# Kernel optimization log

Measured on AMD Instinct MI355X. Metric: run time of the kernel, lower is better.

The kernel has to match this reference:

```python
import jax, jax.numpy as jnp
import numpy as np

B, S, D_IN, H, N_NODES, N_EDGES = 32, 1024, 128, 512, 1024, 16384
SPECTRAL = [0.9, 0.8]   # 0.9 - i*0.1
LEAK = [0.1, 0.15]      # 0.1 + i*0.05
INPUT_SCALING, BIAS_SCALING = 1.0, 0.1


def _make_reservoir(rng, h, radius):
    """Random reservoir matrix with 4-population block scaling, normalized to target spectral radius."""
    W = rng.standard_normal((h, h)).astype(np.float64)
    p = h // 4
    bounds = [0, p, 2 * p, 3 * p, h]
    scales = [(1.2, 0.5), (0.8, 1.3), (1.5, 0.7), (1.0, 1.0)]  # (diag_block, off_block)
    for i in range(4):
        s, e = bounds[i], bounds[i + 1]
        diag, off = scales[i]
        diag_block = W[s:e, s:e] * diag
        W[s:e, :] *= off
        W[s:e, s:e] = diag_block
    ev = np.linalg.eigvals(W)
    W *= radius / np.abs(ev).max()
    return W.astype(np.float32)


def _linear(rng, out_f, in_f):
    k = 1.0 / np.sqrt(in_f)
    Wt = rng.uniform(-k, k, (out_f, in_f)).astype(np.float32)
    b = rng.uniform(-k, k, (out_f,)).astype(np.float32)
    return Wt, b


def setup_inputs() -> dict:
    rng = np.random.default_rng(0)
    x = jnp.asarray(rng.standard_normal((B, S, D_IN)).astype(np.float32))
    edge_index = jnp.asarray(rng.integers(0, N_NODES, (2, N_EDGES)), dtype=jnp.int64)
    inp = {"x": x, "edge_index": edge_index}
    in_sizes = [D_IN, H]
    for l in range(2):
        W_in = (rng.standard_normal((H, in_sizes[l])).astype(np.float32) * INPUT_SCALING)
        W_res = _make_reservoir(rng, H, SPECTRAL[l])
        bias = (rng.standard_normal((H,)).astype(np.float32) * BIAS_SCALING)
        Wp, bp = _linear(rng, N_NODES, H)   # graph_proj: hidden -> num_nodes
        Wu, bu = _linear(rng, H, N_NODES)   # graph_unproj: num_nodes -> hidden
        inp.update({f"W_in{l}": jnp.asarray(W_in), f"W_res{l}": jnp.asarray(W_res),
                    f"bias{l}": jnp.asarray(bias), f"Wp{l}": jnp.asarray(Wp),
                    f"bp{l}": jnp.asarray(bp), f"Wu{l}": jnp.asarray(Wu),
                    f"bu{l}": jnp.asarray(bu)})
    return inp


def _run_layer(x, W_in, W_res, bias, Wp, bp, Wu, bu, src, dst, leak):
    # x: (B, S, D); recurrent scan over time.
    def step(h, x_t):
        inp = x_t @ W_in.T                      # (B, H)
        res = h @ W_res.T                       # (B, H)
        hg = h @ Wp.T + bp                      # (B, N) project onto graph nodes
        # scatter-add message passing: aggr[b, dst] += hg[b, src]
        aggr = jnp.zeros_like(hg).at[:, dst].add(hg[:, src])
        gc = aggr @ Wu.T + bu                   # (B, H)
        h_new = jnp.tanh(inp + res + gc + bias)
        h = (1.0 - leak) * h + leak * h_new     # leaky integration
        return h, h
    h0 = jnp.zeros((x.shape[0], W_res.shape[0]), x.dtype)
    _, ys = jax.lax.scan(step, h0, jnp.swapaxes(x, 0, 1))  # ys: (S, B, H)
    return jnp.swapaxes(ys, 0, 1)


def reference(x, edge_index,
              W_in0, W_res0, bias0, Wp0, bp0, Wu0, bu0,
              W_in1, W_res1, bias1, Wp1, bp1, Wu1, bu1):
    src, dst = edge_index[0], edge_index[1]
    h = _run_layer(x, W_in0, W_res0, bias0, Wp0, bp0, Wu0, bu0, src, dst, LEAK[0])
    h = _run_layer(h, W_in1, W_res1, bias1, Wp1, bp1, Wu1, bu1, src, dst, LEAK[1])
    return h  # dropout is identity in eval mode
```

## Files before the change

### kernel.cpp

```cpp
#include <hip/hip_runtime.h>
#include <hip/hip_bf16.h>
#include <hip/hip_fp16.h>
#include <cstddef>
#include <cstdint>

#define HDIM 512
#define NNODES 1024
#define NEDGES 16384
#define BATCH 32
#define SEQ 1024
#define DIN 128
#define SLICES 8

#define RLX __ATOMIC_RELAXED
#define AGT __HIP_MEMORY_SCOPE_AGENT

typedef _Float16 h2 __attribute__((ext_vector_type(2)));

__global__ void scatter_awp_kernel(const float* __restrict__ Wp,
                                   const int* __restrict__ src,
                                   const int* __restrict__ dst,
                                   float* __restrict__ AWp) {
    int e = blockIdx.x;
    int c = threadIdx.x;
    int s = src[e], d = dst[e];
    atomicAdd(&AWp[d * HDIM + c],       Wp[s * HDIM + c]);
    atomicAdd(&AWp[d * HDIM + 256 + c], Wp[s * HDIM + 256 + c]);
}

__global__ void scatter_abp_kernel(const float* __restrict__ bp,
                                   const int* __restrict__ src,
                                   const int* __restrict__ dst,
                                   float* __restrict__ Abp) {
    int e = blockIdx.x * blockDim.x + threadIdx.x;
    if (e < NEDGES) atomicAdd(&Abp[dst[e]], bp[src[e]]);
}

__global__ void beff_kernel(const float* __restrict__ Wu,
                            const float* __restrict__ Abp,
                            const float* __restrict__ bias,
                            const float* __restrict__ bu,
                            float* __restrict__ beff) {
    int i = threadIdx.x;
    float s = 0.f;
    for (int d = 0; d < NNODES; ++d) s += Wu[i * NNODES + d] * Abp[d];
    beff[i] = bias[i] + bu[i] + s;
}

__global__ void tof16_kernel(const float* __restrict__ in,
                             __half* __restrict__ out, int n) {
    int i = blockIdx.x * blockDim.x + threadIdx.x;
    if (i < n) out[i] = __float2half_rn(in[i]);
}

template <int TB>
__global__ __launch_bounds__(256) void gemm64(const float* __restrict__ A,
                                              const float* __restrict__ B,
                                              float* __restrict__ C,
                                              const float* __restrict__ addend,
                                              int M, int N, int K) {
    const int bn = blockIdx.x, bm = blockIdx.y;
    const int tid = threadIdx.x;
    const int tx = tid & 15, ty = tid >> 4;
    const int m0 = bm * 64, n0 = bn * 64;

    __shared__ float As[16][68];
    __shared__ float Bs[16][68];

    float acc[4][4] = {};

    for (int k0 = 0; k0 < K; k0 += 16) {
        {
            int kk = tid & 15, m = tid >> 4;
            #pragma unroll
            for (int i = 0; i < 4; ++i)
                As[kk][m + 16 * i] = A[(size_t)(m0 + m + 16 * i) * K + k0 + kk];
        }
        if (TB == 0) {
            int n = tid & 63, kk = tid >> 6;
            #pragma unroll
            for (int i = 0; i < 4; ++i)
                Bs[kk + 4 * i][n] = B[(size_t)(k0 + kk + 4 * i) * N + n0 + n];
        } else {
            int kk = tid & 15, n = tid >> 4;
            #pragma unroll
            for (int i = 0; i < 4; ++i)
                Bs[kk][n + 16 * i] = B[(size_t)(n0 + n + 16 * i) * K + k0 + kk];
        }
        __syncthreads();
        #pragma unroll
        for (int kk = 0; kk < 16; ++kk) {
            float4 a4 = *reinterpret_cast<const float4*>(&As[kk][ty * 4]);
            float4 b4 = *reinterpret_cast<const float4*>(&Bs[kk][tx * 4]);
            float av[4] = {a4.x, a4.y, a4.z, a4.w};
            float bv[4] = {b4.x, b4.y, b4.z, b4.w};
            #pragma unroll
            for (int i = 0; i < 4; ++i)
                #pragma unroll
                for (int j = 0; j < 4; ++j)
                    acc[i][j] += av[i] * bv[j];
        }
        __syncthreads();
    }
    #pragma unroll
    for (int i = 0; i < 4; ++i) {
        int m = m0 + ty * 4 + i;
        #pragma unroll
        for (int j = 0; j < 4; ++j) {
            int n = n0 + tx * 4 + j;
            float v = acc[i][j];
            if (addend) v += addend[(size_t)m * N + n];
            C[(size_t)m * N + n] = v;
        }
    }
}

template <int CTRL, int RMASK, bool BC>
__device__ __forceinline__ float dpp_add(float x) {
    int t = __builtin_amdgcn_update_dpp(0, __float_as_int(x), CTRL, RMASK, 0xf, BC);
    return x + __int_as_float(t);
}

__device__ __forceinline__ float reduce32(float x) {
    x = dpp_add<0x111, 0xf, true>(x);
    x = dpp_add<0x112, 0xf, true>(x);
    x = dpp_add<0x114, 0xf, true>(x);
    x = dpp_add<0x118, 0xf, true>(x);
    x = dpp_add<0x142, 0xa, false>(x);
    return x;
}

__device__ __forceinline__ float fast_tanh(float x) {
    float e = __expf(2.0f * x);
    return 1.0f - 2.0f / (e + 1.0f);
}

__device__ __forceinline__ float fdot2(h2 a, h2 b, float c) {
#if __has_builtin(__builtin_amdgcn_fdot2)
    return __builtin_amdgcn_fdot2(a, b, c, false);
#else
    return c + (float)a.x * (float)b.x + (float)a.y * (float)b.y;
#endif
}

__launch_bounds__(512, 1)
__global__ void scan2_kernel(const float* __restrict__ Weff0,
                             const float* __restrict__ beff0,
                             const float* __restrict__ Weff1,
                             const float* __restrict__ beff1,
                             const __half* __restrict__ Win1h,
                             const float* __restrict__ u0,
                             float* __restrict__ out,
                             unsigned long long* __restrict__ hp0,
                             unsigned long long* __restrict__ hp1) {
    const int slice = blockIdx.x;
    const int b = blockIdx.y;
    const int tid = threadIdx.x;
    const int c = tid & 31;
    const int hw = tid >> 5;
    const int rloc = hw * 4;
    const int rowbase = slice * 64 + rloc;
    const bool storer = (c == 31);
    const size_t SLOTS = (size_t)BATCH * HDIM;

    __shared__ __align__(16) __half wl0[64 * HDIM];
    __shared__ __align__(16) __half wl1[64 * HDIM];
    __shared__ __align__(16) __half hs0[2][HDIM];
    __shared__ __align__(16) __half hs1[2][HDIM];

    {
        const float4* s0 = reinterpret_cast<const float4*>(
            Weff0 + (size_t)slice * 64 * HDIM);
        const float4* s1 = reinterpret_cast<const float4*>(
            Weff1 + (size_t)slice * 64 * HDIM);
        h2* d0 = reinterpret_cast<h2*>(wl0);
        h2* d1 = reinterpret_cast<h2*>(wl1);
        #pragma unroll
        for (int i = 0; i < 16; ++i) {
            const int idx = tid + 512 * i;
            float4 v = s0[idx];
            h2 a = {(_Float16)v.x, (_Float16)v.y};
            h2 bb = {(_Float16)v.z, (_Float16)v.w};
            d0[2 * idx] = a;  d0[2 * idx + 1] = bb;
            float4 w = s1[idx];
            h2 e = {(_Float16)w.x, (_Float16)w.y};
            h2 f = {(_Float16)w.z, (_Float16)w.w};
            d1[2 * idx] = e;  d1[2 * idx + 1] = f;
        }
    }

    float4 be04 = make_float4(0.f, 0.f, 0.f, 0.f);
    float4 be14 = make_float4(0.f, 0.f, 0.f, 0.f);
    if (storer) {
        be04 = *reinterpret_cast<const float4*>(beff0 + rowbase);
        be14 = *reinterpret_cast<const float4*>(beff1 + rowbase);
    }
    const float lk0 = 0.10f, olk0 = 0.90f;
    const float lk1 = 0.15f, olk1 = 0.85f;
    const float* u0b = u0 + (size_t)b * SEQ * HDIM;
    float* ob = out + (size_t)b * SEQ * HDIM;
    unsigned long long* h0b = hp0 + (size_t)b * HDIM;
    unsigned long long* h1b = hp1 + (size_t)b * HDIM;
    float4 hold0 = make_float4(0.f, 0.f, 0.f, 0.f);
    float4 hold1 = make_float4(0.f, 0.f, 0.f, 0.f);

    __syncthreads();

    for (int i = 0; i <= SEQ; ++i) {
        h2 wi[4][4][2];
        #pragma unroll
        for (int r = 0; r < 4; ++r) {
            const h2* wp = reinterpret_cast<const h2*>(
                Win1h + (size_t)(rowbase + r) * HDIM);
            #pragma unroll
            for (int k = 0; k < 4; ++k) {
                const int cq = 2 * (c + 32 * k);
                wi[r][k][0] = wp[cq];
                wi[r][k][1] = wp[cq + 1];
            }
        }
        float4 u4 = make_float4(0.f, 0.f, 0.f, 0.f);
        if (storer && i < SEQ)
            u4 = *reinterpret_cast<const float4*>(u0b + (size_t)i * HDIM + rowbase);

        const unsigned long long* sp0 = h0b + (size_t)(i & 1) * SLOTS + tid;
        const unsigned long long* sp1 = h1b + (size_t)((i - 1) & 1) * SLOTS + tid;

        unsigned long long v1 = 0ull;
        if (i >= 1) v1 = __hip_atomic_load(sp1, RLX, AGT);

        unsigned long long v0 = __hip_atomic_load(sp0, RLX, AGT);
        while ((unsigned)(v0 >> 32) != (unsigned)i)
            v0 = __hip_atomic_load(sp0, RLX, AGT);
        hs0[i & 1][tid] = __float2half(__uint_as_float((unsigned)v0));
        __syncthreads();

        if (i < SEQ) {
            float a0 = 0.f, a1 = 0.f, a2 = 0.f, a3 = 0.f;
            const h2* hv = reinterpret_cast<const h2*>(&hs0[i & 1][0]);
            #pragma unroll
            for (int k = 0; k < 4; ++k) {
                const int cq = 2 * (c + 32 * k);
                h2 ha = hv[cq], hb = hv[cq + 1];
                const h2* w0 = reinterpret_cast<const h2*>(wl0) + (rloc + 0) * 256 + cq;
                const h2* w1 = reinterpret_cast<const h2*>(wl0) + (rloc + 1) * 256 + cq;
                const h2* w2 = reinterpret_cast<const h2*>(wl0) + (rloc + 2) * 256 + cq;
                const h2* w3 = reinterpret_cast<const h2*>(wl0) + (rloc + 3) * 256 + cq;
                a0 = fdot2(w0[0], ha, a0); a0 = fdot2(w0[1], hb, a0);
                a1 = fdot2(w1[0], ha, a1); a1 = fdot2(w1[1], hb, a1);
                a2 = fdot2(w2[0], ha, a2); a2 = fdot2(w2[1], hb, a2);
                a3 = fdot2(w3[0], ha, a3); a3 = fdot2(w3[1], hb, a3);
            }
            a0 = reduce32(a0);
            a1 = reduce32(a1);
            a2 = reduce32(a2);
            a3 = reduce32(a3);
            if (storer) {
                float n0 = olk0 * hold0.x + lk0 * fast_tanh(a0 + u4.x + be04.x);
                float n1 = olk0 * hold0.y + lk0 * fast_tanh(a1 + u4.y + be04.y);
                float n2 = olk0 * hold0.z + lk0 * fast_tanh(a2 + u4.z + be04.z);
                float n3 = olk0 * hold0.w + lk0 * fast_tanh(a3 + u4.w + be04.w);
                hold0 = make_float4(n0, n1, n2, n3);
                unsigned long long tg = ((unsigned long long)(unsigned)(i + 1)) << 32;
                unsigned long long* hp = h0b + (size_t)((i + 1) & 1) * SLOTS + rowbase;
                __hip_atomic_store(hp + 0, tg | __float_as_uint(n0), RLX, AGT);
                __hip_atomic_store(hp + 1, tg | __float_as_uint(n1), RLX, AGT);
                __hip_atomic_store(hp + 2, tg | __float_as_uint(n2), RLX, AGT);
                __hip_atomic_store(hp + 3, tg | __float_as_uint(n3), RLX, AGT);
            }
        }

        if (i >= 1) {
            while ((unsigned)(v1 >> 32) != (unsigned)(i - 1))
                v1 = __hip_atomic_load(sp1, RLX, AGT);
            hs1[(i - 1) & 1][tid] = __float2half(__uint_as_float((unsigned)v1));
        }
        __syncthreads();

        if (i >= 1) {
            float g0 = 0.f, g1 = 0.f, g2 = 0.f, g3 = 0.f;
            const h2* pv = reinterpret_cast<const h2*>(&hs0[i & 1][0]);
            const h2* qv = reinterpret_cast<const h2*>(&hs1[(i - 1) & 1][0]);
            #pragma unroll
            for (int k = 0; k < 4; ++k) {
                const int cq = 2 * (c + 32 * k);
                h2 pa = pv[cq], pb = pv[cq + 1];
                h2 qa = qv[cq], qb = qv[cq + 1];
                const h2* e0 = reinterpret_cast<const h2*>(wl1) + (rloc + 0) * 256 + cq;
                const h2* e1 = reinterpret_cast<const h2*>(wl1) + (rloc + 1) * 256 + cq;
                const h2* e2 = reinterpret_cast<const h2*>(wl1) + (rloc + 2) * 256 + cq;
                const h2* e3 = reinterpret_cast<const h2*>(wl1) + (rloc + 3) * 256 + cq;
                g0 = fdot2(wi[0][k][0], pa, g0); g0 = fdot2(wi[0][k][1], pb, g0);
                g0 = fdot2(e0[0], qa, g0);       g0 = fdot2(e0[1], qb, g0);
                g1 = fdot2(wi[1][k][0], pa, g1); g1 = fdot2(wi[1][k][1], pb, g1);
                g1 = fdot2(e1[0], qa, g1);       g1 = fdot2(e1[1], qb, g1);
                g2 = fdot2(wi[2][k][0], pa, g2); g2 = fdot2(wi[2][k][1], pb, g2);
                g2 = fdot2(e2[0], qa, g2);       g2 = fdot2(e2[1], qb, g2);
                g3 = fdot2(wi[3][k][0], pa, g3); g3 = fdot2(wi[3][k][1], pb, g3);
                g3 = fdot2(e3[0], qa, g3);       g3 = fdot2(e3[1], qb, g3);
            }
            g0 = reduce32(g0);
            g1 = reduce32(g1);
            g2 = reduce32(g2);
            g3 = reduce32(g3);
            if (storer) {
                float m0 = olk1 * hold1.x + lk1 * fast_tanh(g0 + be14.x);
                float m1 = olk1 * hold1.y + lk1 * fast_tanh(g1 + be14.y);
                float m2 = olk1 * hold1.z + lk1 * fast_tanh(g2 + be14.z);
                float m3 = olk1 * hold1.w + lk1 * fast_tanh(g3 + be14.w);
                hold1 = make_float4(m0, m1, m2, m3);
                unsigned long long tg = ((unsigned long long)(unsigned)i) << 32;
                unsigned long long* hp = h1b + (size_t)(i & 1) * SLOTS + rowbase;
                __hip_atomic_store(hp + 0, tg | __float_as_uint(m0), RLX, AGT);
                __hip_atomic_store(hp + 1, tg | __float_as_uint(m1), RLX, AGT);
                __hip_atomic_store(hp + 2, tg | __float_as_uint(m2), RLX, AGT);
                __hip_atomic_store(hp + 3, tg | __float_as_uint(m3), RLX, AGT);
                *reinterpret_cast<float4*>(ob + (size_t)(i - 1) * HDIM + rowbase) =
                    make_float4(m0, m1, m2, m3);
            }
        }
    }
}

extern "C" void kernel_launch(void* const* d_in, const int* in_sizes, int n_in,
                              void* d_out, int out_size, void* d_ws, size_t ws_size,
                              hipStream_t stream) {
    const float* x      = (const float*)d_in[0];
    const int*   edges  = (const int*)d_in[1];
    const float* W_in0  = (const float*)d_in[2];
    const float* W_res0 = (const float*)d_in[3];
    const float* bias0  = (const float*)d_in[4];
    const float* Wp0    = (const float*)d_in[5];
    const float* bp0    = (const float*)d_in[6];
    const float* Wu0    = (const float*)d_in[7];
    const float* bu0    = (const float*)d_in[8];
    const float* W_in1  = (const float*)d_in[9];
    const float* W_res1 = (const float*)d_in[10];
    const float* bias1  = (const float*)d_in[11];
    const float* Wp1    = (const float*)d_in[12];
    const float* bp1    = (const float*)d_in[13];
    const float* Wu1    = (const float*)d_in[14];
    const float* bu1    = (const float*)d_in[15];

    const int* src = edges;
    const int* dst = edges + NEDGES;
    float* out = (float*)d_out;

    char* base = (char*)d_ws;
    float* ws_u = (float*)base;
    char* q = base + (size_t)67108864;
    float* AWp = (float*)q;
    unsigned long long* hp0 = (unsigned long long*)q;
    unsigned long long* hp1 = (unsigned long long*)(q + 262144);
    __half* Win1h = (__half*)(q + 524288);
    char* p2 = q + 2097152;
    float* Abp   = (float*)p2;
    float* Weff0 = (float*)(p2 + 4096);
    float* Weff1 = (float*)(p2 + 1052672);
    float* beff0 = (float*)(p2 + 2101248);
    float* beff1 = (float*)(p2 + 2103296);

    hipMemsetAsync(AWp, 0, 2097152, stream);
    hipMemsetAsync(Abp, 0, 4096, stream);
    scatter_awp_kernel<<<NEDGES, 256, 0, stream>>>(Wp0, src, dst, AWp);
    scatter_abp_kernel<<<NEDGES / 256, 256, 0, stream>>>(bp0, src, dst, Abp);
    gemm64<0><<<dim3(8, 8), 256, 0, stream>>>(Wu0, AWp, Weff0, W_res0, 512, 512, 1024);
    beff_kernel<<<1, 512, 0, stream>>>(Wu0, Abp, bias0, bu0, beff0);

    hipMemsetAsync(AWp, 0, 2097152, stream);
    hipMemsetAsync(Abp, 0, 4096, stream);
    scatter_awp_kernel<<<NEDGES, 256, 0, stream>>>(Wp1, src, dst, AWp);
    scatter_abp_kernel<<<NEDGES / 256, 256, 0, stream>>>(bp1, src, dst, Abp);
    gemm64<0><<<dim3(8, 8), 256, 0, stream>>>(Wu1, AWp, Weff1, W_res1, 512, 512, 1024);
    beff_kernel<<<1, 512, 0, stream>>>(Wu1, Abp, bias1, bu1, beff1);

    gemm64<1><<<dim3(512 / 64, 32768 / 64), 256, 0, stream>>>(
        x, W_in0, ws_u, nullptr, BATCH * SEQ, HDIM, DIN);

    hipMemsetAsync(q, 0, 524288, stream);
    tof16_kernel<<<HDIM * HDIM / 1024, 1024, 0, stream>>>(W_in1, Win1h, HDIM * HDIM);

    scan2_kernel<<<dim3(SLICES, BATCH), 512, 0, stream>>>(
        Weff0, beff0, Weff1, beff1, Win1h, ws_u, out, hp0, hp1);
}
```

Measured before the change: 3.448 ms.

## Pack two fp16 hidden values per flag slot and overlap W_in1 dot with polling

The cross-block hidden-state exchange now packs two fp16 values plus a step tag into each 64-bit slot. This halves the number of slots each block polls and writes, and only 256 threads poll instead of 512. The layer-1 input projection (W_in1 · h0) is moved ahead of the wait on layer-1 state, so that compute overlaps the spin-wait. The polling loop also keeps a second load in flight. The cost is that exchanged values are rounded to fp16 before exchange, which the old code already did on read, so accuracy is essentially unchanged.

```diff
diff --git a/kernel.cpp b/kernel.cpp
--- a/kernel.cpp
+++ b/kernel.cpp
@@ -11,11 +11,17 @@
 #define SEQ 1024
 #define DIN 128
 #define SLICES 8
+#define PSLOT (BATCH * 256)
 
 #define RLX __ATOMIC_RELAXED
 #define AGT __HIP_MEMORY_SCOPE_AGENT
 
 typedef _Float16 h2 __attribute__((ext_vector_type(2)));
+
+__device__ __forceinline__ unsigned pk(float a, float b) {
+    h2 v = {(_Float16)a, (_Float16)b};
+    return __builtin_bit_cast(unsigned, v);
+}
 
 __global__ void scatter_awp_kernel(const float* __restrict__ Wp,
                                    const int* __restrict__ src,
@@ -161,7 +167,7 @@
     const int rloc = hw * 4;
     const int rowbase = slice * 64 + rloc;
     const bool storer = (c == 31);
-    const size_t SLOTS = (size_t)BATCH * HDIM;
+    const bool poller = (tid < 256);
 
     __shared__ __align__(16) __half wl0[64 * HDIM];
     __shared__ __align__(16) __half wl1[64 * HDIM];
@@ -179,13 +185,11 @@
         for (int i = 0; i < 16; ++i) {
             const int idx = tid + 512 * i;
             float4 v = s0[idx];
-            h2 a = {(_Float16)v.x, (_Float16)v.y};
-            h2 bb = {(_Float16)v.z, (_Float16)v.w};
-            d0[2 * idx] = a;  d0[2 * idx + 1] = bb;
+            d0[2 * idx]     = h2{(_Float16)v.x, (_Float16)v.y};
+            d0[2 * idx + 1] = h2{(_Float16)v.z, (_Float16)v.w};
             float4 w = s1[idx];
-            h2 e = {(_Float16)w.x, (_Float16)w.y};
-            h2 f = {(_Float16)w.z, (_Float16)w.w};
-            d1[2 * idx] = e;  d1[2 * idx + 1] = f;
+            d1[2 * idx]     = h2{(_Float16)w.x, (_Float16)w.y};
+            d1[2 * idx + 1] = h2{(_Float16)w.z, (_Float16)w.w};
         }
     }
 
@@ -199,8 +203,9 @@
     const float lk1 = 0.15f, olk1 = 0.85f;
     const float* u0b = u0 + (size_t)b * SEQ * HDIM;
     float* ob = out + (size_t)b * SEQ * HDIM;
-    unsigned long long* h0b = hp0 + (size_t)b * HDIM;
-    unsigned long long* h1b = hp1 + (size_t)b * HDIM;
+    unsigned long long* h0b = hp0 + (size_t)b * 256;
+    unsigned long long* h1b = hp1 + (size_t)b * 256;
+    const int pslot = slice * 32 + hw * 2;
     float4 hold0 = make_float4(0.f, 0.f, 0.f, 0.f);
     float4 hold1 = make_float4(0.f, 0.f, 0.f, 0.f);
 
@@ -223,16 +228,22 @@
         if (storer && i < SEQ)
             u4 = *reinterpret_cast<const float4*>(u0b + (size_t)i * HDIM + rowbase);
 
-        const unsigned long long* sp0 = h0b + (size_t)(i & 1) * SLOTS + tid;
-        const unsigned long long* sp1 = h1b + (size_t)((i - 1) & 1) * SLOTS + tid;
+        const unsigned long long* sp0 = h0b + (size_t)(i & 1) * PSLOT + tid;
+        const unsigned long long* sp1 = h1b + (size_t)((i - 1) & 1) * PSLOT + tid;
 
         unsigned long long v1 = 0ull;
-        if (i >= 1) v1 = __hip_atomic_load(sp1, RLX, AGT);
-
-        unsigned long long v0 = __hip_atomic_load(sp0, RLX, AGT);
-        while ((unsigned)(v0 >> 32) != (unsigned)i)
-            v0 = __hip_atomic_load(sp0, RLX, AGT);
-        hs0[i & 1][tid] = __float2half(__uint_as_float((unsigned)v0));
+        if (poller && i >= 1) v1 = __hip_atomic_load(sp1, RLX, AGT);
+
+        if (poller) {
+            unsigned long long v0 = __hip_atomic_load(sp0, RLX, AGT);
+            unsigned long long vb = __hip_atomic_load(sp0, RLX, AGT);
+            while ((unsigned)(v0 >> 32) != (unsigned)i) {
+                v0 = vb;
+                vb = __hip_atomic_load(sp0, RLX, AGT);
+            }
+            reinterpret_cast<h2*>(&hs0[i & 1][0])[tid] =
+                __builtin_bit_cast(h2, (unsigned)v0);
+        }
         __syncthreads();
 
         if (i < SEQ) {
@@ -262,42 +273,50 @@
                 float n3 = olk0 * hold0.w + lk0 * fast_tanh(a3 + u4.w + be04.w);
                 hold0 = make_float4(n0, n1, n2, n3);
                 unsigned long long tg = ((unsigned long long)(unsigned)(i + 1)) << 32;
-                unsigned long long* hp = h0b + (size_t)((i + 1) & 1) * SLOTS + rowbase;
-                __hip_atomic_store(hp + 0, tg | __float_as_uint(n0), RLX, AGT);
-                __hip_atomic_store(hp + 1, tg | __float_as_uint(n1), RLX, AGT);
-                __hip_atomic_store(hp + 2, tg | __float_as_uint(n2), RLX, AGT);
-                __hip_atomic_store(hp + 3, tg | __float_as_uint(n3), RLX, AGT);
-            }
-        }
-
+                unsigned long long* hp = h0b + (size_t)((i + 1) & 1) * PSLOT + pslot;
+                __hip_atomic_store(hp + 0, tg | pk(n0, n1), RLX, AGT);
+                __hip_atomic_store(hp + 1, tg | pk(n2, n3), RLX, AGT);
+            }
+        }
+
+        float g0 = 0.f, g1 = 0.f, g2 = 0.f, g3 = 0.f;
         if (i >= 1) {
-            while ((unsigned)(v1 >> 32) != (unsigned)(i - 1))
-                v1 = __hip_atomic_load(sp1, RLX, AGT);
-            hs1[(i - 1) & 1][tid] = __float2half(__uint_as_float((unsigned)v1));
-        }
-        __syncthreads();
-
-        if (i >= 1) {
-            float g0 = 0.f, g1 = 0.f, g2 = 0.f, g3 = 0.f;
             const h2* pv = reinterpret_cast<const h2*>(&hs0[i & 1][0]);
-            const h2* qv = reinterpret_cast<const h2*>(&hs1[(i - 1) & 1][0]);
             #pragma unroll
             for (int k = 0; k < 4; ++k) {
                 const int cq = 2 * (c + 32 * k);
                 h2 pa = pv[cq], pb = pv[cq + 1];
+                g0 = fdot2(wi[0][k][0], pa, g0); g0 = fdot2(wi[0][k][1], pb, g0);
+                g1 = fdot2(wi[1][k][0], pa, g1); g1 = fdot2(wi[1][k][1], pb, g1);
+                g2 = fdot2(wi[2][k][0], pa, g2); g2 = fdot2(wi[2][k][1], pb, g2);
+                g3 = fdot2(wi[3][k][0], pa, g3); g3 = fdot2(wi[3][k][1], pb, g3);
+            }
+            if (poller) {
+                unsigned long long vb = __hip_atomic_load(sp1, RLX, AGT);
+                while ((unsigned)(v1 >> 32) != (unsigned)(i - 1)) {
+                    v1 = vb;
+                    vb = __hip_atomic_load(sp1, RLX, AGT);
+                }
+                reinterpret_cast<h2*>(&hs1[(i - 1) & 1][0])[tid] =
+                    __builtin_bit_cast(h2, (unsigned)v1);
+            }
+        }
+        __syncthreads();
+
+        if (i >= 1) {
+            const h2* qv = reinterpret_cast<const h2*>(&hs1[(i - 1) & 1][0]);
+            #pragma unroll
+            for (int k = 0; k < 4; ++k) {
+                const int cq = 2 * (c + 32 * k);
                 h2 qa = qv[cq], qb = qv[cq + 1];
                 const h2* e0 = reinterpret_cast<const h2*>(wl1) + (rloc + 0) * 256 + cq;
                 const h2* e1 = reinterpret_cast<const h2*>(wl1) + (rloc + 1) * 256 + cq;
                 const h2* e2 = reinterpret_cast<const h2*>(wl1) + (rloc + 2) * 256 + cq;
                 const h2* e3 = reinterpret_cast<const h2*>(wl1) + (rloc + 3) * 256 + cq;
-                g0 = fdot2(wi[0][k][0], pa, g0); g0 = fdot2(wi[0][k][1], pb, g0);
-                g0 = fdot2(e0[0], qa, g0);       g0 = fdot2(e0[1], qb, g0);
-                g1 = fdot2(wi[1][k][0], pa, g1); g1 = fdot2(wi[1][k][1], pb, g1);
-                g1 = fdot2(e1[0], qa, g1);       g1 = fdot2(e1[1], qb, g1);
-                g2 = fdot2(wi[2][k][0], pa, g2); g2 = fdot2(wi[2][k][1], pb, g2);
-                g2 = fdot2(e2[0], qa, g2);       g2 = fdot2(e2[1], qb, g2);
-                g3 = fdot2(wi[3][k][0], pa, g3); g3 = fdot2(wi[3][k][1], pb, g3);
-                g3 = fdot2(e3[0], qa, g3);       g3 = fdot2(e3[1], qb, g3);
+                g0 = fdot2(e0[0], qa, g0); g0 = fdot2(e0[1], qb, g0);
+                g1 = fdot2(e1[0], qa, g1); g1 = fdot2(e1[1], qb, g1);
+                g2 = fdot2(e2[0], qa, g2); g2 = fdot2(e2[1], qb, g2);
+                g3 = fdot2(e3[0], qa, g3); g3 = fdot2(e3[1], qb, g3);
             }
             g0 = reduce32(g0);
             g1 = reduce32(g1);
@@ -310,11 +329,9 @@
                 float m3 = olk1 * hold1.w + lk1 * fast_tanh(g3 + be14.w);
                 hold1 = make_float4(m0, m1, m2, m3);
                 unsigned long long tg = ((unsigned long long)(unsigned)i) << 32;
-                unsigned long long* hp = h1b + (size_t)(i & 1) * SLOTS + rowbase;
-                __hip_atomic_store(hp + 0, tg | __float_as_uint(m0), RLX, AGT);
-                __hip_atomic_store(hp + 1, tg | __float_as_uint(m1), RLX, AGT);
-                __hip_atomic_store(hp + 2, tg | __float_as_uint(m2), RLX, AGT);
-                __hip_atomic_store(hp + 3, tg | __float_as_uint(m3), RLX, AGT);
+                unsigned long long* hp = h1b + (size_t)(i & 1) * PSLOT + pslot;
+                __hip_atomic_store(hp + 0, tg | pk(m0, m1), RLX, AGT);
+                __hip_atomic_store(hp + 1, tg | pk(m2, m3), RLX, AGT);
                 *reinterpret_cast<float4*>(ob + (size_t)(i - 1) * HDIM + rowbase) =
                     make_float4(m0, m1, m2, m3);
             }
@@ -351,8 +368,8 @@
     char* q = base + (size_t)67108864;
     float* AWp = (float*)q;
     unsigned long long* hp0 = (unsigned long long*)q;
-    unsigned long long* hp1 = (unsigned long long*)(q + 262144);
-    __half* Win1h = (__half*)(q + 524288);
+    unsigned long long* hp1 = (unsigned long long*)(q + 131072);
+    __half* Win1h = (__half*)(q + 262144);
     char* p2 = q + 2097152;
     float* Abp   = (float*)p2;
     float* Weff0 = (float*)(p2 + 4096);
@@ -377,7 +394,7 @@
     gemm64<1><<<dim3(512 / 64, 32768 / 64), 256, 0, stream>>>(
         x, W_in0, ws_u, nullptr, BATCH * SEQ, HDIM, DIN);
 
-    hipMemsetAsync(q, 0, 524288, stream);
+    hipMemsetAsync(q, 0, 262144, stream);
     tof16_kernel<<<HDIM * HDIM / 1024, 1024, 0, stream>>>(W_in1, Win1h, HDIM * HDIM);
 
     scan2_kernel<<<dim3(SLICES, BATCH), 512, 0, stream>>>(
```

Result: faster. 3.379 ms (-2.0%).
